# Kernel optimization log

Hardware: AMD Instinct MI355X
Metric: run time of the kernel (lower is better)

## Reference

```python
import jax, jax.numpy as jnp
import numpy as np

K_NN = 64          # ume_knn
RADIUS = 1.5       # ume_desc_rad
EPS_M = 1e-6
EPS_T = 1e-16


def ball_query_idx(kp, pts, K, radius):
    # kp: [bs, n_kp, 3], pts: [bs, N, 3] -> idx [bs, n_kp, K], -1 padded
    N = pts.shape[1]
    d2 = jnp.sum((kp[:, :, None, :] - pts[:, None, :, :]) ** 2, axis=-1)  # [bs,n_kp,N]
    mask = d2 < radius ** 2
    cand = jnp.where(mask, jnp.arange(N, dtype=jnp.int32), N)
    order = jnp.sort(cand, axis=-1)[..., :K]          # first K in-ball indices (by point index)
    return jnp.where(order == N, -1, order)


def ball_query_gather(pts, idx):
    # pad row 0 with zeros so idx=-1 gathers zeros (matches torch ball_query_gather)
    bs = pts.shape[0]
    padded = jnp.concatenate([jnp.zeros((bs, 1, pts.shape[-1]), pts.dtype), pts], axis=1)
    return padded[jnp.arange(bs)[:, None, None], idx + 1]  # [bs, n_kp, K, D]


def ume_mat(points, features):
    # points: [B', K, 3], features: [B', K, F] -> [B', F, 4]
    m0 = jnp.sum(features, axis=1)                       # [B', F]
    m1 = jnp.einsum('bkf,bkd->bfd', features, points)    # [B', F, 3]
    um = jnp.concatenate([m0[:, :, None], m1], axis=2)   # [B', F, 4]
    denom = jnp.sum(m0, axis=-1)[:, None, None] + EPS_M  # [B',1,1]
    return um / denom


def batch_estimate_transform_ume(G, H):
    # G, H: [B, F, 4]
    mg, mh = G[:, :, 0:1], H[:, :, 0:1]                  # [B,F,1]
    g, h = G[:, :, 1:], H[:, :, 1:]                      # [B,F,3]
    mg_sq = jnp.sum(mg ** 2, axis=1, keepdims=True) + EPS_T
    mg_mh = jnp.sum(mg * mh, axis=1, keepdims=True)
    gmg = jnp.sum(g * mg, axis=1, keepdims=True)         # [B,1,3]
    hmg = jnp.sum(h * mg, axis=1, keepdims=True)
    wlc = gmg / (mg_sq + EPS_T)
    wrc = hmg / (mg_mh + EPS_T)
    left = g - wlc * mg
    right = h - wrc * mh
    M = jnp.einsum('bfi,bfj->bij', right, left)          # right^T @ left, [B,3,3]
    U, S, VH = jnp.linalg.svd(jnp.swapaxes(M, 1, 2))
    sgn = jnp.sign(jnp.linalg.det(U @ VH))
    qd = jnp.stack([jnp.ones_like(sgn), jnp.ones_like(sgn), sgn], axis=-1)  # diag(1,1,sgn)
    R = (U * qd[:, None, :]) @ VH                        # [B,3,3]
    b2 = (wrc - wlc @ R)[:, 0, :]                        # [B,3]
    H_orth = jnp.linalg.qr(H, mode='reduced')[0]
    G_orth = jnp.linalg.qr(G, mode='reduced')[0]
    diff = H_orth @ jnp.swapaxes(H_orth, 1, 2) - G_orth @ jnp.swapaxes(G_orth, 1, 2)
    D = 0.707 * jnp.sqrt(jnp.sum(diff ** 2, axis=(1, 2)))
    top = jnp.concatenate([jnp.swapaxes(R, 1, 2), b2[:, :, None]], axis=2)  # [B,3,4]
    bottom = jnp.broadcast_to(jnp.array([[0.0, 0.0, 0.0, 1.0]], G.dtype), (G.shape[0], 1, 4))
    T = jnp.concatenate([top, bottom], axis=1)           # [B,4,4]
    return T, D


def setup_inputs() -> dict:
    key = jax.random.key(0)
    ks = jax.random.split(key, 6)
    bs, N, F, n_kp = 2, 16384, 64, 64
    return {
        'source_points': jax.random.normal(ks[0], (bs, N, 3), jnp.float32),
        'source_features': jax.random.uniform(ks[1], (bs, N, F), jnp.float32),
        'source_kp': jax.random.normal(ks[2], (bs, n_kp, 3), jnp.float32),
        'target_points': jax.random.normal(ks[3], (bs, N, 3), jnp.float32),
        'target_features': jax.random.uniform(ks[4], (bs, N, F), jnp.float32),
        'target_kp': jax.random.normal(ks[5], (bs, n_kp, 3), jnp.float32),
    }


def reference(source_points, source_features, source_kp, target_points, target_features, target_kp):
    bs, n_kp = source_kp.shape[0], source_kp.shape[1]
    F = source_features.shape[-1]
    s_idx = ball_query_idx(source_kp, source_points, K_NN, RADIUS)
    t_idx = ball_query_idx(target_kp, target_points, K_NN, RADIUS)
    s_pts = ball_query_gather(source_points, s_idx).reshape(bs * n_kp, K_NN, 3)
    s_ft = ball_query_gather(source_features, s_idx).reshape(bs * n_kp, K_NN, F)
    t_pts = ball_query_gather(target_points, t_idx).reshape(bs * n_kp, K_NN, 3)
    t_ft = ball_query_gather(target_features, t_idx).reshape(bs * n_kp, K_NN, F)
    G_kp = ume_mat(s_pts, s_ft).reshape(bs, n_kp, F, 4)[:, :, None]   # [bs,n_kp,1,F,4]
    H_kp = ume_mat(t_pts, t_ft).reshape(bs, n_kp, F, 4)[:, None]      # [bs,1,n_kp,F,4]
    G = jnp.broadcast_to(G_kp, (bs, n_kp, n_kp, F, 4)).reshape(-1, F, 4)
    H = jnp.broadcast_to(H_kp, (bs, n_kp, n_kp, F, 4)).reshape(-1, F, 4)
    T, D = batch_estimate_transform_ume(G, H)
    T = T.reshape(bs, n_kp, n_kp, 4, 4)
    D = D.reshape(bs, n_kp, n_kp)
    return T, D, jnp.squeeze(G_kp), jnp.squeeze(H_kp)
```

## Files before the change

kernel.cpp:

```cpp
#include <hip/hip_runtime.h>
#include <math.h>

#define N_PTS 16384
#define N_KP  64
#define NF    64
#define KNN   64
#define NWAVE 16

#define OFF_T 0
#define OFF_D 131072
#define OFF_G 139264
#define OFF_H 172032

__device__ __forceinline__ float wsum(float v) {
  #pragma unroll
  for (int m = 1; m < 64; m <<= 1) v += __shfl_xor(v, m, 64);
  return v;
}

__global__ __launch_bounds__(1024) void ume_stage1(
    const float* __restrict__ sp, const float* __restrict__ sf, const float* __restrict__ skp,
    const float* __restrict__ tp, const float* __restrict__ tf, const float* __restrict__ tkp,
    float* __restrict__ out, double* __restrict__ rec)
{
  const int kp = blockIdx.x, b = blockIdx.y, side = blockIdx.z;
  const int tid  = threadIdx.x;
  const int lane = tid & 63;
  const int w    = tid >> 6;
  const float* pts  = side ? tp  : sp;
  const float* feat = side ? tf  : sf;
  const float* kps  = side ? tkp : skp;

  const float kx = kps[(b*N_KP + kp)*3 + 0];
  const float ky = kps[(b*N_KP + kp)*3 + 1];
  const float kz = kps[(b*N_KP + kp)*3 + 2];

  __shared__ int   s_widx[NWAVE*KNN];
  __shared__ float s_wpx[NWAVE*KNN], s_wpy[NWAVE*KNN], s_wpz[NWAVE*KNN];
  __shared__ int   s_wcount[NWAVE];
  __shared__ int   s_final[KNN];
  __shared__ float s_px[KNN], s_py[KNN], s_pz[KNN];
  __shared__ float s_m0[NWAVE][NF], s_mx[NWAVE][NF], s_my[NWAVE][NF], s_mz[NWAVE][NF];

  int base_total = 0;

  for (int round = 0; round < 16; ++round) {
    const int p = round*1024 + w*64 + lane;
    const float* pp = pts + ((size_t)b*N_PTS + p)*3;
    const float dx = pp[0]-kx, dy = pp[1]-ky, dz = pp[2]-kz;
    const bool hit = (dx*dx + dy*dy + dz*dz) < 2.25f;
    const unsigned long long m = __ballot(hit);
    if (hit) {
      const int pos = __popcll(m & ((1ull<<lane)-1ull));
      s_widx[w*KNN + pos] = p;
      s_wpx[w*KNN + pos] = pp[0]; s_wpy[w*KNN + pos] = pp[1]; s_wpz[w*KNN + pos] = pp[2];
    }
    if (lane == 0) s_wcount[w] = (int)__popcll(m);
    __syncthreads();

    int myoff = base_total, newtotal = base_total;
    #pragma unroll
    for (int q = 0; q < NWAVE; ++q) {
      const int cq = s_wcount[q];
      if (q < w) myoff += cq;
      newtotal += cq;
    }
    if (newtotal > KNN) newtotal = KNN;

    if (lane < s_wcount[w]) {
      const int slot = myoff + lane;
      if (slot < KNN) {
        s_final[slot] = s_widx[w*KNN + lane];
        s_px[slot] = s_wpx[w*KNN + lane];
        s_py[slot] = s_wpy[w*KNN + lane];
        s_pz[slot] = s_wpz[w*KNN + lane];
      }
    }
    base_total = newtotal;
    __syncthreads();

    if (base_total >= KNN) break;
  }

  const int total = base_total;

  {
    const int f = tid & 63, g = tid >> 6;
    float m0 = 0.f, mxv = 0.f, myv = 0.f, mzv = 0.f;
    #pragma unroll
    for (int t = 0; t < 4; ++t) {
      const int k = g + t*NWAVE;
      if (k < total) {
        const float fv = feat[((size_t)b*N_PTS + s_final[k])*NF + f];
        m0  += fv;
        mxv += fv * s_px[k];
        myv += fv * s_py[k];
        mzv += fv * s_pz[k];
      }
    }
    s_m0[g][f] = m0; s_mx[g][f] = mxv; s_my[g][f] = myv; s_mz[g][f] = mzv;
  }
  __syncthreads();

  if (tid >= 64) return;

  float m0 = 0.f, mxv = 0.f, myv = 0.f, mzv = 0.f;
  #pragma unroll
  for (int g = 0; g < NWAVE; ++g) {
    m0  += s_m0[g][lane];
    mxv += s_mx[g][lane];
    myv += s_my[g][lane];
    mzv += s_mz[g][lane];
  }
  const float denom = wsum(m0) + 1e-6f;
  float u[4];
  u[0] = m0/denom; u[1] = mxv/denom; u[2] = myv/denom; u[3] = mzv/denom;

  float* dst = out + (side ? OFF_H : OFF_G) + ((size_t)(b*N_KP+kp)*NF + lane)*4;
  dst[0]=u[0]; dst[1]=u[1]; dst[2]=u[2]; dst[3]=u[3];

  float A[4][4];
  #pragma unroll
  for (int c = 0; c < 4; ++c)
    #pragma unroll
    for (int d = c; d < 4; ++d) {
      const float s = wsum(u[c]*u[d]);
      A[c][d] = s; A[d][c] = s;
    }

  if (lane < 16)
    rec[(size_t)((side*2 + b)*N_KP + kp)*16 + lane] = (double)A[lane>>2][lane&3];
}

__device__ __forceinline__ void chol_inv4(const double A[4][4], double Ai[4][4], double sc[4]) {
  #pragma unroll
  for (int c = 0; c < 4; ++c) sc[c] = 1.0/sqrt(fmax(A[c][c], 1e-300));
  double Ah[4][4];
  #pragma unroll
  for (int c = 0; c < 4; ++c)
    #pragma unroll
    for (int d = 0; d < 4; ++d) Ah[c][d] = A[c][d]*sc[c]*sc[d];
  double L[4][4] = {};
  for (int c = 0; c < 4; ++c) {
    double dv = Ah[c][c];
    for (int k = 0; k < c; ++k) dv -= L[c][k]*L[c][k];
    dv = sqrt(fmax(dv, 1e-14));
    L[c][c] = dv;
    for (int r = c+1; r < 4; ++r) {
      double v = Ah[r][c];
      for (int k = 0; k < c; ++k) v -= L[r][k]*L[c][k];
      L[r][c] = v/dv;
    }
  }
  double Li[4][4] = {};
  for (int c = 0; c < 4; ++c) {
    Li[c][c] = 1.0/L[c][c];
    for (int r = c+1; r < 4; ++r) {
      double s = 0.0;
      for (int k = c; k < r; ++k) s += L[r][k]*Li[k][c];
      Li[r][c] = -s/L[r][r];
    }
  }
  for (int r = 0; r < 4; ++r)
    for (int c = 0; c < 4; ++c) {
      double s = 0.0;
      for (int k = 0; k < 4; ++k) s += Li[k][r]*Li[k][c];
      Ai[r][c] = s;
    }
}

__global__ __launch_bounds__(64) void ume_stage2(
    const float* __restrict__ gh, float* __restrict__ out,
    const double* __restrict__ rec)
{
  const int jt = blockIdx.x, it = blockIdx.y, b = blockIdx.z;
  const int lane = threadIdx.x;
  const int i = it*8 + (lane >> 3);
  const int j = jt*8 + (lane & 7);

  const float4* Gp = (const float4*)(gh + OFF_G) + (size_t)(b*N_KP + i)*NF;
  const float4* Hp = (const float4*)(gh + OFF_H) + (size_t)(b*N_KP + j)*NF;

  double X[4][4] = {};
  for (int f = 0; f < NF; ++f) {
    const float4 g = Gp[f];
    const float4 h = Hp[f];
    const double gc[4] = {(double)g.x, (double)g.y, (double)g.z, (double)g.w};
    const double hc[4] = {(double)h.x, (double)h.y, (double)h.z, (double)h.w};
    #pragma unroll
    for (int c = 0; c < 4; ++c)
      #pragma unroll
      for (int d = 0; d < 4; ++d)
        X[c][d] += hc[c]*gc[d];
  }

  double Ag[4][4], Bh[4][4];
  {
    const double* pg = rec + (size_t)(b*N_KP + i)*16;
    const double* ph = rec + (size_t)((2 + b)*N_KP + j)*16;
    #pragma unroll
    for (int k = 0; k < 16; ++k) { Ag[k>>2][k&3] = pg[k]; Bh[k>>2][k&3] = ph[k]; }
  }
  double Aig[4][4], scg[4], Bih[4][4], sch[4];
  chol_inv4(Ag, Aig, scg);
  chol_inv4(Bh, Bih, sch);

  const double dwl = Ag[0][0] + 2e-16;
  const double wl[3] = {Ag[0][1]/dwl, Ag[0][2]/dwl, Ag[0][3]/dwl};
  const double dmm = X[0][0] + 1e-16;
  double wr[3];
  wr[0] = X[1][0]/dmm; wr[1] = X[2][0]/dmm; wr[2] = X[3][0]/dmm;

  double M[3][3];
  #pragma unroll
  for (int r = 0; r < 3; ++r)
    #pragma unroll
    for (int c = 0; c < 3; ++c)
      M[r][c] = X[1+r][1+c] - wl[c]*X[1+r][0] - wr[r]*X[0][1+c] + wr[r]*wl[c]*X[0][0];

  double C[3][3];
  for (int r = 0; r < 3; ++r)
    for (int c = 0; c < 3; ++c) C[r][c] = M[c][r];

  double mmax = 0.0;
  for (int r = 0; r < 3; ++r)
    for (int c = 0; c < 3; ++c) mmax = fmax(mmax, fabs(C[r][c]));

  double R[3][3] = {{1,0,0},{0,1,0},{0,0,1}};
  if (mmax > 1e-300) {
    const double is = 1.0/mmax;
    for (int r = 0; r < 3; ++r)
      for (int c = 0; c < 3; ++c) C[r][c] *= is;
    double K[3][3];
    for (int p = 0; p < 3; ++p)
      for (int q = 0; q < 3; ++q) {
        double s = 0.0;
        for (int r = 0; r < 3; ++r) s += C[r][p]*C[r][q];
        K[p][q] = s;
      }
    double V[3][3] = {{1,0,0},{0,1,0},{0,0,1}};
    for (int sweep = 0; sweep < 5; ++sweep) {
      for (int p = 0; p < 2; ++p)
        for (int q = p+1; q < 3; ++q) {
          const double apq = K[p][q];
          if (fabs(apq) < 1e-60) continue;
          const double tau = (K[q][q] - K[p][p])/(2.0*apq);
          const double t   = (tau >= 0.0 ? 1.0 : -1.0)/(fabs(tau) + sqrt(1.0 + tau*tau));
          const double cth = 1.0/sqrt(1.0 + t*t);
          const double sth = t*cth;
          for (int k = 0; k < 3; ++k) {
            const double a = K[p][k], bb_ = K[q][k];
            K[p][k] = cth*a - sth*bb_;
            K[q][k] = sth*a + cth*bb_;
          }
          for (int k = 0; k < 3; ++k) {
            const double a = K[k][p], bb_ = K[k][q];
            K[k][p] = cth*a - sth*bb_;
            K[k][q] = sth*a + cth*bb_;
          }
          for (int k = 0; k < 3; ++k) {
            const double a = V[k][p], bb_ = V[k][q];
            V[k][p] = cth*a - sth*bb_;
            V[k][q] = sth*a + cth*bb_;
          }
        }
    }
    int o0 = 0, o1 = 1, o2 = 2;
    double e0 = K[0][0], e1 = K[1][1], e2 = K[2][2];
    if (e0 < e1) { double te=e0; e0=e1; e1=te; int to=o0; o0=o1; o1=to; }
    if (e0 < e2) { double te=e0; e0=e2; e2=te; int to=o0; o0=o2; o2=to; }
    if (e1 < e2) { double te=e1; e1=e2; e2=te; int to=o1; o1=o2; o2=to; }
    (void)e0; (void)e1; (void)e2;
    double v1[3] = {V[0][o0], V[1][o0], V[2][o0]};
    double v2[3] = {V[0][o1], V[1][o1], V[2][o1]};
    double u1[3], u2[3];
    for (int r = 0; r < 3; ++r) u1[r] = C[r][0]*v1[0] + C[r][1]*v1[1] + C[r][2]*v1[2];
    const double n1 = sqrt(u1[0]*u1[0] + u1[1]*u1[1] + u1[2]*u1[2]);
    if (n1 > 1e-150) { u1[0]/=n1; u1[1]/=n1; u1[2]/=n1; }
    else             { u1[0]=1.0; u1[1]=0.0; u1[2]=0.0; }
    for (int r = 0; r < 3; ++r) u2[r] = C[r][0]*v2[0] + C[r][1]*v2[1] + C[r][2]*v2[2];
    const double d12 = u2[0]*u1[0] + u2[1]*u1[1] + u2[2]*u1[2];
    for (int r = 0; r < 3; ++r) u2[r] -= d12*u1[r];
    const double n2 = sqrt(u2[0]*u2[0] + u2[1]*u2[1] + u2[2]*u2[2]);
    if (n2 > 1e-100) { u2[0]/=n2; u2[1]/=n2; u2[2]/=n2; }
    else {
      double t0, t1, t2;
      if (fabs(u1[0]) < 0.9) { t0=1.0; t1=0.0; t2=0.0; } else { t0=0.0; t1=1.0; t2=0.0; }
      const double dd = t0*u1[0] + t1*u1[1] + t2*u1[2];
      u2[0]=t0-dd*u1[0]; u2[1]=t1-dd*u1[1]; u2[2]=t2-dd*u1[2];
      const double nn = sqrt(u2[0]*u2[0] + u2[1]*u2[1] + u2[2]*u2[2]);
      u2[0]/=nn; u2[1]/=nn; u2[2]/=nn;
    }
    const double u3[3] = {u1[1]*u2[2]-u1[2]*u2[1], u1[2]*u2[0]-u1[0]*u2[2], u1[0]*u2[1]-u1[1]*u2[0]};
    const double v3[3] = {v1[1]*v2[2]-v1[2]*v2[1], v1[2]*v2[0]-v1[0]*v2[2], v1[0]*v2[1]-v1[1]*v2[0]};
    for (int r = 0; r < 3; ++r)
      for (int c = 0; c < 3; ++c)
        R[r][c] = u1[r]*v1[c] + u2[r]*v2[c] + u3[r]*v3[c];
  }

  double bb[3];
  for (int d = 0; d < 3; ++d)
    bb[d] = wr[d] - (wl[0]*R[0][d] + wl[1]*R[1][d] + wl[2]*R[2][d]);

  double Xh[4][4];
  for (int c = 0; c < 4; ++c)
    for (int d = 0; d < 4; ++d) Xh[c][d] = X[c][d]*sch[c]*scg[d];
  double W[4][4];
  for (int r = 0; r < 4; ++r)
    for (int c = 0; c < 4; ++c) {
      double s = 0.0;
      for (int k = 0; k < 4; ++k) s += Bih[r][k]*Xh[k][c];
      W[r][c] = s;
    }
  double tr = 0.0;
  for (int r = 0; r < 4; ++r)
    for (int c = 0; c < 4; ++c) {
      double s = 0.0;
      for (int k = 0; k < 4; ++k) s += W[r][k]*Aig[k][c];
      tr += s*Xh[r][c];
    }
  const double Dv = 0.707*sqrt(fmax(8.0 - 2.0*tr, 0.0));

  float* tptr = out + OFF_T + (size_t)((b*N_KP + i)*N_KP + j)*16;
  tptr[0]=(float)R[0][0];  tptr[1]=(float)R[1][0];  tptr[2]=(float)R[2][0];  tptr[3]=(float)bb[0];
  tptr[4]=(float)R[0][1];  tptr[5]=(float)R[1][1];  tptr[6]=(float)R[2][1];  tptr[7]=(float)bb[1];
  tptr[8]=(float)R[0][2];  tptr[9]=(float)R[1][2];  tptr[10]=(float)R[2][2]; tptr[11]=(float)bb[2];
  tptr[12]=0.f; tptr[13]=0.f; tptr[14]=0.f; tptr[15]=1.f;

  out[OFF_D + (size_t)(b*N_KP + i)*N_KP + j] = (float)Dv;
}

extern "C" void kernel_launch(void* const* d_in, const int* in_sizes, int n_in,
                              void* d_out, int out_size, void* d_ws, size_t ws_size,
                              hipStream_t stream) {
  const float* sp  = (const float*)d_in[0];
  const float* sf  = (const float*)d_in[1];
  const float* skp = (const float*)d_in[2];
  const float* tp  = (const float*)d_in[3];
  const float* tf  = (const float*)d_in[4];
  const float* tkp = (const float*)d_in[5];
  float* out = (float*)d_out;
  double* rec = (double*)d_ws;

  dim3 gA(N_KP, 2, 2);
  ume_stage1<<<gA, 1024, 0, stream>>>(sp, sf, skp, tp, tf, tkp, out, rec);
  dim3 gB(8, 8, 2);
  ume_stage2<<<gB, 64, 0, stream>>>(out, out, rec);
}
```

Baseline: 117.7 us.

## Fuse both stages into one kernel with a grid barrier and restructure ball query

Merges the ball-query/UME stage and the pairwise transform stage into a single kernel synchronised by a global atomic barrier, removing one kernel launch. The ball query now has each wave scan its own contiguous 1024-point chunk with all loads issued up front, replacing the 16 block-wide synchronised rounds and their early exit. The Cholesky-based 4x4 inverse becomes a cofactor inverse, and several divisions become reciprocal multiplies. The spin barrier depends on all 256 blocks being co-resident and adds a memset launch, and the per-wave scan always reads every point even when the first 64 hits are found early.

```diff
diff --git a/kernel.cpp b/kernel.cpp
--- a/kernel.cpp
+++ b/kernel.cpp
@@ -12,16 +12,59 @@
 #define OFF_G 139264
 #define OFF_H 172032
 
+#define BARRIER_BYTE_OFF 65536
+#define NBLOCKS 256u
+
 __device__ __forceinline__ float wsum(float v) {
   #pragma unroll
   for (int m = 1; m < 64; m <<= 1) v += __shfl_xor(v, m, 64);
   return v;
 }
 
-__global__ __launch_bounds__(1024) void ume_stage1(
+__device__ __forceinline__ void cof_inv4(const double A[4][4], double Ai[4][4], double sc[4]) {
+  #pragma unroll
+  for (int c = 0; c < 4; ++c) sc[c] = 1.0/sqrt(fmax(A[c][c], 1e-300));
+  double M[4][4];
+  #pragma unroll
+  for (int r = 0; r < 4; ++r)
+    #pragma unroll
+    for (int c = 0; c < 4; ++c) M[r][c] = A[r][c]*sc[r]*sc[c];
+  const double s0 = M[0][0]*M[1][1] - M[0][1]*M[1][0];
+  const double s1 = M[0][0]*M[1][2] - M[0][2]*M[1][0];
+  const double s2 = M[0][0]*M[1][3] - M[0][3]*M[1][0];
+  const double s3 = M[0][1]*M[1][2] - M[0][2]*M[1][1];
+  const double s4 = M[0][1]*M[1][3] - M[0][3]*M[1][1];
+  const double s5 = M[0][2]*M[1][3] - M[0][3]*M[1][2];
+  const double c5 = M[2][2]*M[3][3] - M[2][3]*M[3][2];
+  const double c4 = M[2][1]*M[3][3] - M[2][3]*M[3][1];
+  const double c3 = M[2][1]*M[3][2] - M[2][2]*M[3][1];
+  const double c2 = M[2][0]*M[3][3] - M[2][3]*M[3][0];
+  const double c1 = M[2][0]*M[3][2] - M[2][2]*M[3][0];
+  const double c0 = M[2][0]*M[3][1] - M[2][1]*M[3][0];
+  const double det = s0*c5 - s1*c4 + s2*c3 + s3*c2 - s4*c1 + s5*c0;
+  const double invd = 1.0/fmax(det, 1e-300);
+  Ai[0][0] = ( M[1][1]*c5 - M[1][2]*c4 + M[1][3]*c3)*invd;
+  Ai[0][1] = (-M[0][1]*c5 + M[0][2]*c4 - M[0][3]*c3)*invd;
+  Ai[0][2] = ( M[3][1]*s5 - M[3][2]*s4 + M[3][3]*s3)*invd;
+  Ai[0][3] = (-M[2][1]*s5 + M[2][2]*s4 - M[2][3]*s3)*invd;
+  Ai[1][0] = (-M[1][0]*c5 + M[1][2]*c2 - M[1][3]*c1)*invd;
+  Ai[1][1] = ( M[0][0]*c5 - M[0][2]*c2 + M[0][3]*c1)*invd;
+  Ai[1][2] = (-M[3][0]*s5 + M[3][2]*s2 - M[3][3]*s1)*invd;
+  Ai[1][3] = ( M[2][0]*s5 - M[2][2]*s2 + M[2][3]*s1)*invd;
+  Ai[2][0] = ( M[1][0]*c4 - M[1][1]*c2 + M[1][3]*c0)*invd;
+  Ai[2][1] = (-M[0][0]*c4 + M[0][1]*c2 - M[0][3]*c0)*invd;
+  Ai[2][2] = ( M[3][0]*s4 - M[3][1]*s2 + M[3][3]*s0)*invd;
+  Ai[2][3] = (-M[2][0]*s4 + M[2][1]*s2 - M[2][3]*s0)*invd;
+  Ai[3][0] = (-M[1][0]*c3 + M[1][1]*c1 - M[1][2]*c0)*invd;
+  Ai[3][1] = ( M[0][0]*c3 - M[0][1]*c1 + M[0][2]*c0)*invd;
+  Ai[3][2] = (-M[3][0]*s3 + M[3][1]*s1 - M[3][2]*s0)*invd;
+  Ai[3][3] = ( M[2][0]*s3 - M[2][1]*s1 + M[2][2]*s0)*invd;
+}
+
+__global__ __launch_bounds__(1024, 4) void ume_fused(
     const float* __restrict__ sp, const float* __restrict__ sf, const float* __restrict__ skp,
     const float* __restrict__ tp, const float* __restrict__ tf, const float* __restrict__ tkp,
-    float* __restrict__ out, double* __restrict__ rec)
+    float* __restrict__ out, double* __restrict__ rec, unsigned int* __restrict__ bar)
 {
   const int kp = blockIdx.x, b = blockIdx.y, side = blockIdx.z;
   const int tid  = threadIdx.x;
@@ -42,50 +85,55 @@
   __shared__ float s_px[KNN], s_py[KNN], s_pz[KNN];
   __shared__ float s_m0[NWAVE][NF], s_mx[NWAVE][NF], s_my[NWAVE][NF], s_mz[NWAVE][NF];
 
-  int base_total = 0;
-
-  for (int round = 0; round < 16; ++round) {
-    const int p = round*1024 + w*64 + lane;
-    const float* pp = pts + ((size_t)b*N_PTS + p)*3;
-    const float dx = pp[0]-kx, dy = pp[1]-ky, dz = pp[2]-kz;
-    const bool hit = (dx*dx + dy*dy + dz*dz) < 2.25f;
-    const unsigned long long m = __ballot(hit);
-    if (hit) {
-      const int pos = __popcll(m & ((1ull<<lane)-1ull));
-      s_widx[w*KNN + pos] = p;
-      s_wpx[w*KNN + pos] = pp[0]; s_wpy[w*KNN + pos] = pp[1]; s_wpz[w*KNN + pos] = pp[2];
-    }
-    if (lane == 0) s_wcount[w] = (int)__popcll(m);
-    __syncthreads();
-
-    int myoff = base_total, newtotal = base_total;
-    #pragma unroll
-    for (int q = 0; q < NWAVE; ++q) {
-      const int cq = s_wcount[q];
-      if (q < w) myoff += cq;
-      newtotal += cq;
-    }
-    if (newtotal > KNN) newtotal = KNN;
-
-    if (lane < s_wcount[w]) {
-      const int slot = myoff + lane;
-      if (slot < KNN) {
-        s_final[slot] = s_widx[w*KNN + lane];
-        s_px[slot] = s_wpx[w*KNN + lane];
-        s_py[slot] = s_wpy[w*KNN + lane];
-        s_pz[slot] = s_wpz[w*KNN + lane];
+  {
+    const float* base = pts + ((size_t)b*N_PTS + w*1024 + lane)*3;
+    float px[16], py[16], pz[16];
+    #pragma unroll
+    for (int k = 0; k < 16; ++k) {
+      const float* pp = base + (size_t)k*192;
+      px[k] = pp[0]; py[k] = pp[1]; pz[k] = pp[2];
+    }
+    int running = 0;
+    #pragma unroll
+    for (int k = 0; k < 16; ++k) {
+      const float dx = px[k]-kx, dy = py[k]-ky, dz = pz[k]-kz;
+      const bool hit = (dx*dx + dy*dy + dz*dz) < 2.25f;
+      const unsigned long long m = __ballot(hit);
+      if (hit) {
+        const int pos = running + __popcll(m & ((1ull<<lane)-1ull));
+        if (pos < KNN) {
+          s_widx[w*KNN + pos] = w*1024 + k*64 + lane;
+          s_wpx[w*KNN + pos] = px[k]; s_wpy[w*KNN + pos] = py[k]; s_wpz[w*KNN + pos] = pz[k];
+        }
       }
-    }
-    base_total = newtotal;
-    __syncthreads();
-
-    if (base_total >= KNN) break;
-  }
-
-  const int total = base_total;
+      running += (int)__popcll(m);
+    }
+    if (lane == 0) s_wcount[w] = running > KNN ? KNN : running;
+  }
+  __syncthreads();
+
+  int myoff = 0, total = 0;
+  #pragma unroll
+  for (int q = 0; q < NWAVE; ++q) {
+    const int cq = s_wcount[q];
+    if (q < w) myoff += cq;
+    total += cq;
+  }
+  if (total > KNN) total = KNN;
+
+  if (lane < s_wcount[w]) {
+    const int slot = myoff + lane;
+    if (slot < KNN) {
+      s_final[slot] = s_widx[w*KNN + lane];
+      s_px[slot] = s_wpx[w*KNN + lane];
+      s_py[slot] = s_wpy[w*KNN + lane];
+      s_pz[slot] = s_wpz[w*KNN + lane];
+    }
+  }
+  __syncthreads();
 
   {
-    const int f = tid & 63, g = tid >> 6;
+    const int f = lane, g = w;
     float m0 = 0.f, mxv = 0.f, myv = 0.f, mzv = 0.f;
     #pragma unroll
     for (int t = 0; t < 4; ++t) {
@@ -102,86 +150,55 @@
   }
   __syncthreads();
 
-  if (tid >= 64) return;
-
-  float m0 = 0.f, mxv = 0.f, myv = 0.f, mzv = 0.f;
-  #pragma unroll
-  for (int g = 0; g < NWAVE; ++g) {
-    m0  += s_m0[g][lane];
-    mxv += s_mx[g][lane];
-    myv += s_my[g][lane];
-    mzv += s_mz[g][lane];
-  }
-  const float denom = wsum(m0) + 1e-6f;
-  float u[4];
-  u[0] = m0/denom; u[1] = mxv/denom; u[2] = myv/denom; u[3] = mzv/denom;
-
-  float* dst = out + (side ? OFF_H : OFF_G) + ((size_t)(b*N_KP+kp)*NF + lane)*4;
-  dst[0]=u[0]; dst[1]=u[1]; dst[2]=u[2]; dst[3]=u[3];
-
-  float A[4][4];
-  #pragma unroll
-  for (int c = 0; c < 4; ++c)
-    #pragma unroll
-    for (int d = c; d < 4; ++d) {
-      const float s = wsum(u[c]*u[d]);
-      A[c][d] = s; A[d][c] = s;
-    }
-
-  if (lane < 16)
-    rec[(size_t)((side*2 + b)*N_KP + kp)*16 + lane] = (double)A[lane>>2][lane&3];
-}
-
-__device__ __forceinline__ void chol_inv4(const double A[4][4], double Ai[4][4], double sc[4]) {
-  #pragma unroll
-  for (int c = 0; c < 4; ++c) sc[c] = 1.0/sqrt(fmax(A[c][c], 1e-300));
-  double Ah[4][4];
-  #pragma unroll
-  for (int c = 0; c < 4; ++c)
-    #pragma unroll
-    for (int d = 0; d < 4; ++d) Ah[c][d] = A[c][d]*sc[c]*sc[d];
-  double L[4][4] = {};
-  for (int c = 0; c < 4; ++c) {
-    double dv = Ah[c][c];
-    for (int k = 0; k < c; ++k) dv -= L[c][k]*L[c][k];
-    dv = sqrt(fmax(dv, 1e-14));
-    L[c][c] = dv;
-    for (int r = c+1; r < 4; ++r) {
-      double v = Ah[r][c];
-      for (int k = 0; k < c; ++k) v -= L[r][k]*L[c][k];
-      L[r][c] = v/dv;
-    }
-  }
-  double Li[4][4] = {};
-  for (int c = 0; c < 4; ++c) {
-    Li[c][c] = 1.0/L[c][c];
-    for (int r = c+1; r < 4; ++r) {
-      double s = 0.0;
-      for (int k = c; k < r; ++k) s += L[r][k]*Li[k][c];
-      Li[r][c] = -s/L[r][r];
-    }
-  }
-  for (int r = 0; r < 4; ++r)
-    for (int c = 0; c < 4; ++c) {
-      double s = 0.0;
-      for (int k = 0; k < 4; ++k) s += Li[k][r]*Li[k][c];
-      Ai[r][c] = s;
-    }
-}
-
-__global__ __launch_bounds__(64) void ume_stage2(
-    const float* __restrict__ gh, float* __restrict__ out,
-    const double* __restrict__ rec)
-{
-  const int jt = blockIdx.x, it = blockIdx.y, b = blockIdx.z;
-  const int lane = threadIdx.x;
-  const int i = it*8 + (lane >> 3);
-  const int j = jt*8 + (lane & 7);
-
-  const float4* Gp = (const float4*)(gh + OFF_G) + (size_t)(b*N_KP + i)*NF;
-  const float4* Hp = (const float4*)(gh + OFF_H) + (size_t)(b*N_KP + j)*NF;
+  if (tid < 64) {
+    float m0 = 0.f, mxv = 0.f, myv = 0.f, mzv = 0.f;
+    #pragma unroll
+    for (int g = 0; g < NWAVE; ++g) {
+      m0  += s_m0[g][lane];
+      mxv += s_mx[g][lane];
+      myv += s_my[g][lane];
+      mzv += s_mz[g][lane];
+    }
+    const float denom = wsum(m0) + 1e-6f;
+    float u[4];
+    u[0] = m0/denom; u[1] = mxv/denom; u[2] = myv/denom; u[3] = mzv/denom;
+
+    float* dst = out + (side ? OFF_H : OFF_G) + ((size_t)(b*N_KP+kp)*NF + lane)*4;
+    dst[0]=u[0]; dst[1]=u[1]; dst[2]=u[2]; dst[3]=u[3];
+
+    float A[4][4];
+    #pragma unroll
+    for (int c = 0; c < 4; ++c)
+      #pragma unroll
+      for (int d = c; d < 4; ++d) {
+        const float s = wsum(u[c]*u[d]);
+        A[c][d] = s; A[d][c] = s;
+      }
+    if (lane < 16)
+      rec[(size_t)((side*2 + b)*N_KP + kp)*16 + lane] = (double)A[lane>>2][lane&3];
+  }
+
+  __threadfence();
+  __syncthreads();
+  if (tid == 0) {
+    __hip_atomic_fetch_add(bar, 1u, __ATOMIC_ACQ_REL, __HIP_MEMORY_SCOPE_AGENT);
+    while (__hip_atomic_load(bar, __ATOMIC_ACQUIRE, __HIP_MEMORY_SCOPE_AGENT) < NBLOCKS)
+      __builtin_amdgcn_s_sleep(2);
+  }
+  __syncthreads();
+
+  if (tid >= 32) return;
+  const int bid = kp + N_KP*(b + 2*side);
+  const int q   = bid*32 + tid;
+  const int b2  = q >> 12;
+  const int i   = (q >> 6) & 63;
+  const int j   = q & 63;
+
+  const float4* Gp = (const float4*)(out + OFF_G) + (size_t)(b2*N_KP + i)*NF;
+  const float4* Hp = (const float4*)(out + OFF_H) + (size_t)(b2*N_KP + j)*NF;
 
   double X[4][4] = {};
+  #pragma unroll 4
   for (int f = 0; f < NF; ++f) {
     const float4 g = Gp[f];
     const float4 h = Hp[f];
@@ -196,31 +213,30 @@
 
   double Ag[4][4], Bh[4][4];
   {
-    const double* pg = rec + (size_t)(b*N_KP + i)*16;
-    const double* ph = rec + (size_t)((2 + b)*N_KP + j)*16;
+    const double* pg = rec + (size_t)(b2*N_KP + i)*16;
+    const double* ph = rec + (size_t)((2 + b2)*N_KP + j)*16;
     #pragma unroll
     for (int k = 0; k < 16; ++k) { Ag[k>>2][k&3] = pg[k]; Bh[k>>2][k&3] = ph[k]; }
   }
   double Aig[4][4], scg[4], Bih[4][4], sch[4];
-  chol_inv4(Ag, Aig, scg);
-  chol_inv4(Bh, Bih, sch);
-
-  const double dwl = Ag[0][0] + 2e-16;
-  const double wl[3] = {Ag[0][1]/dwl, Ag[0][2]/dwl, Ag[0][3]/dwl};
-  const double dmm = X[0][0] + 1e-16;
-  double wr[3];
-  wr[0] = X[1][0]/dmm; wr[1] = X[2][0]/dmm; wr[2] = X[3][0]/dmm;
-
-  double M[3][3];
+  cof_inv4(Ag, Aig, scg);
+  cof_inv4(Bh, Bih, sch);
+
+  const double inv_dwl = 1.0/(Ag[0][0] + 2e-16);
+  const double wl[3] = {Ag[0][1]*inv_dwl, Ag[0][2]*inv_dwl, Ag[0][3]*inv_dwl};
+  const double inv_dmm = 1.0/(X[0][0] + 1e-16);
+  const double wr[3] = {X[1][0]*inv_dmm, X[2][0]*inv_dmm, X[3][0]*inv_dmm};
+
+  double M3[3][3];
   #pragma unroll
   for (int r = 0; r < 3; ++r)
     #pragma unroll
     for (int c = 0; c < 3; ++c)
-      M[r][c] = X[1+r][1+c] - wl[c]*X[1+r][0] - wr[r]*X[0][1+c] + wr[r]*wl[c]*X[0][0];
+      M3[r][c] = X[1+r][1+c] - wl[c]*X[1+r][0] - wr[r]*X[0][1+c] + wr[r]*wl[c]*X[0][0];
 
   double C[3][3];
   for (int r = 0; r < 3; ++r)
-    for (int c = 0; c < 3; ++c) C[r][c] = M[c][r];
+    for (int c = 0; c < 3; ++c) C[r][c] = M3[c][r];
 
   double mmax = 0.0;
   for (int r = 0; r < 3; ++r)
@@ -233,35 +249,35 @@
       for (int c = 0; c < 3; ++c) C[r][c] *= is;
     double K[3][3];
     for (int p = 0; p < 3; ++p)
-      for (int q = 0; q < 3; ++q) {
+      for (int qq = 0; qq < 3; ++qq) {
         double s = 0.0;
-        for (int r = 0; r < 3; ++r) s += C[r][p]*C[r][q];
-        K[p][q] = s;
+        for (int r = 0; r < 3; ++r) s += C[r][p]*C[r][qq];
+        K[p][qq] = s;
       }
     double V[3][3] = {{1,0,0},{0,1,0},{0,0,1}};
     for (int sweep = 0; sweep < 5; ++sweep) {
       for (int p = 0; p < 2; ++p)
-        for (int q = p+1; q < 3; ++q) {
-          const double apq = K[p][q];
-          if (fabs(apq) < 1e-60) continue;
-          const double tau = (K[q][q] - K[p][p])/(2.0*apq);
+        for (int qq = p+1; qq < 3; ++qq) {
+          const double apq = K[p][qq];
+          if (apq*apq < 1e-26) continue;
+          const double tau = (K[qq][qq] - K[p][p])/(2.0*apq);
           const double t   = (tau >= 0.0 ? 1.0 : -1.0)/(fabs(tau) + sqrt(1.0 + tau*tau));
           const double cth = 1.0/sqrt(1.0 + t*t);
           const double sth = t*cth;
           for (int k = 0; k < 3; ++k) {
-            const double a = K[p][k], bb_ = K[q][k];
+            const double a = K[p][k], bb_ = K[qq][k];
             K[p][k] = cth*a - sth*bb_;
-            K[q][k] = sth*a + cth*bb_;
+            K[qq][k] = sth*a + cth*bb_;
           }
           for (int k = 0; k < 3; ++k) {
-            const double a = K[k][p], bb_ = K[k][q];
+            const double a = K[k][p], bb_ = K[k][qq];
             K[k][p] = cth*a - sth*bb_;
-            K[k][q] = sth*a + cth*bb_;
+            K[k][qq] = sth*a + cth*bb_;
           }
           for (int k = 0; k < 3; ++k) {
-            const double a = V[k][p], bb_ = V[k][q];
+            const double a = V[k][p], bb_ = V[k][qq];
             V[k][p] = cth*a - sth*bb_;
-            V[k][q] = sth*a + cth*bb_;
+            V[k][qq] = sth*a + cth*bb_;
           }
         }
     }
@@ -276,20 +292,20 @@
     double u1[3], u2[3];
     for (int r = 0; r < 3; ++r) u1[r] = C[r][0]*v1[0] + C[r][1]*v1[1] + C[r][2]*v1[2];
     const double n1 = sqrt(u1[0]*u1[0] + u1[1]*u1[1] + u1[2]*u1[2]);
-    if (n1 > 1e-150) { u1[0]/=n1; u1[1]/=n1; u1[2]/=n1; }
+    if (n1 > 1e-150) { const double rn = 1.0/n1; u1[0]*=rn; u1[1]*=rn; u1[2]*=rn; }
     else             { u1[0]=1.0; u1[1]=0.0; u1[2]=0.0; }
     for (int r = 0; r < 3; ++r) u2[r] = C[r][0]*v2[0] + C[r][1]*v2[1] + C[r][2]*v2[2];
     const double d12 = u2[0]*u1[0] + u2[1]*u1[1] + u2[2]*u1[2];
     for (int r = 0; r < 3; ++r) u2[r] -= d12*u1[r];
     const double n2 = sqrt(u2[0]*u2[0] + u2[1]*u2[1] + u2[2]*u2[2]);
-    if (n2 > 1e-100) { u2[0]/=n2; u2[1]/=n2; u2[2]/=n2; }
+    if (n2 > 1e-100) { const double rn = 1.0/n2; u2[0]*=rn; u2[1]*=rn; u2[2]*=rn; }
     else {
       double t0, t1, t2;
       if (fabs(u1[0]) < 0.9) { t0=1.0; t1=0.0; t2=0.0; } else { t0=0.0; t1=1.0; t2=0.0; }
       const double dd = t0*u1[0] + t1*u1[1] + t2*u1[2];
       u2[0]=t0-dd*u1[0]; u2[1]=t1-dd*u1[1]; u2[2]=t2-dd*u1[2];
-      const double nn = sqrt(u2[0]*u2[0] + u2[1]*u2[1] + u2[2]*u2[2]);
-      u2[0]/=nn; u2[1]/=nn; u2[2]/=nn;
+      const double nn = 1.0/sqrt(u2[0]*u2[0] + u2[1]*u2[1] + u2[2]*u2[2]);
+      u2[0]*=nn; u2[1]*=nn; u2[2]*=nn;
     }
     const double u3[3] = {u1[1]*u2[2]-u1[2]*u2[1], u1[2]*u2[0]-u1[0]*u2[2], u1[0]*u2[1]-u1[1]*u2[0]};
     const double v3[3] = {v1[1]*v2[2]-v1[2]*v2[1], v1[2]*v2[0]-v1[0]*v2[2], v1[0]*v2[1]-v1[1]*v2[0]};
@@ -321,13 +337,13 @@
     }
   const double Dv = 0.707*sqrt(fmax(8.0 - 2.0*tr, 0.0));
 
-  float* tptr = out + OFF_T + (size_t)((b*N_KP + i)*N_KP + j)*16;
+  float* tptr = out + OFF_T + (size_t)((b2*N_KP + i)*N_KP + j)*16;
   tptr[0]=(float)R[0][0];  tptr[1]=(float)R[1][0];  tptr[2]=(float)R[2][0];  tptr[3]=(float)bb[0];
   tptr[4]=(float)R[0][1];  tptr[5]=(float)R[1][1];  tptr[6]=(float)R[2][1];  tptr[7]=(float)bb[1];
   tptr[8]=(float)R[0][2];  tptr[9]=(float)R[1][2];  tptr[10]=(float)R[2][2]; tptr[11]=(float)bb[2];
   tptr[12]=0.f; tptr[13]=0.f; tptr[14]=0.f; tptr[15]=1.f;
 
-  out[OFF_D + (size_t)(b*N_KP + i)*N_KP + j] = (float)Dv;
+  out[OFF_D + (size_t)(b2*N_KP + i)*N_KP + j] = (float)Dv;
 }
 
 extern "C" void kernel_launch(void* const* d_in, const int* in_sizes, int n_in,
@@ -341,9 +357,9 @@
   const float* tkp = (const float*)d_in[5];
   float* out = (float*)d_out;
   double* rec = (double*)d_ws;
-
-  dim3 gA(N_KP, 2, 2);
-  ume_stage1<<<gA, 1024, 0, stream>>>(sp, sf, skp, tp, tf, tkp, out, rec);
-  dim3 gB(8, 8, 2);
-  ume_stage2<<<gB, 64, 0, stream>>>(out, out, rec);
+  unsigned int* bar = (unsigned int*)((char*)d_ws + BARRIER_BYTE_OFF);
+
+  hipMemsetAsync(bar, 0, 64, stream);
+  dim3 g(N_KP, 2, 2);
+  ume_fused<<<g, 1024, 0, stream>>>(sp, sf, skp, tp, tf, tkp, out, rec, bar);
 }
```

Result: slower. 177.2 us (+50.5%).
